# Kernel tuning notes

Hardware: AMD Instinct MI355X
Metric: run time of the kernel (lower is better)

## Reference

```python
import jax, jax.numpy as jnp
import numpy as np

B, S, H, I, E, TOP_K = 2, 1024, 1024, 2048, 8, 2


def setup_inputs() -> dict:
    key = jax.random.key(0)
    ks = jax.random.split(key, 5)
    return {
        "hidden_states": jax.random.normal(ks[0], (B, S, H), jnp.float32),
        # torch Linear weights are (out, in)
        "router_w": jax.random.normal(ks[1], (E, H), jnp.float32) * 0.02,
        "w1": jax.random.normal(ks[2], (E, I, H), jnp.float32) * 0.02,
        "v": jax.random.normal(ks[3], (E, I, H), jnp.float32) * 0.02,
        "w2": jax.random.normal(ks[4], (E, H, I), jnp.float32) * 0.02,
    }


def _moe(x, router_w, w1, v, w2):
    # x: [T, H] flattened tokens
    T = x.shape[0]
    n_exp = router_w.shape[0]
    logits = x @ router_w.T                                    # [T, E]
    probs = jax.nn.softmax(logits.astype(jnp.float32), axis=-1)
    top_p, top_i = jax.lax.top_k(probs, TOP_K)                 # [T, K]
    top_p = top_p / top_p.sum(axis=-1, keepdims=True)
    top_p = top_p.astype(x.dtype)
    # dense gate matrix [T, E]; zero for unselected experts -> identical math
    # to the torch gather / index_add combine
    gates = jnp.zeros((T, n_exp), x.dtype).at[
        jnp.arange(T)[:, None], top_i].set(top_p)
    out = jnp.zeros_like(x)
    for e in range(n_exp):  # small fixed expert loop keeps peak memory low
        h = jax.nn.gelu(x @ w1[e].T, approximate=False) * (x @ v[e].T)  # [T, I]
        out = out + gates[:, e:e + 1] * (h @ w2[e].T)                   # [T, H]
    return out, logits


def reference(hidden_states, router_w, w1, v, w2):
    b, s, h = hidden_states.shape
    out, logits = _moe(hidden_states.reshape(-1, h), router_w, w1, v, w2)
    return out.reshape(b, s, h), logits
```

## Files before the change

### kernel.cpp

```cpp
#include <hip/hip_runtime.h>
#include <math.h>

#define T 2048
#define HD 1024
#define ID 2048
#define NE 8
#define CSTRIDE 32

typedef short bf16x8 __attribute__((ext_vector_type(8)));
typedef float f32x4 __attribute__((ext_vector_type(4)));
typedef unsigned short u16x4 __attribute__((ext_vector_type(4)));

__device__ __forceinline__ unsigned short f2bf(float f) {
  union { float f; unsigned u; } v; v.f = f;
  unsigned r = v.u + 0x7FFFu + ((v.u >> 16) & 1u);
  return (unsigned short)(r >> 16);
}

__device__ __forceinline__ void cast_chunk16(const float* __restrict__ s,
                                             unsigned short* __restrict__ d,
                                             size_t base) {
  size_t o = base + (size_t)threadIdx.x * 4;
#pragma unroll
  for (int k = 0; k < 4; k++) {
    float4 f = *(const float4*)(s + o + k * 1024);
    u16x4 h;
    h[0] = f2bf(f.x); h[1] = f2bf(f.y); h[2] = f2bf(f.z); h[3] = f2bf(f.w);
    *(u16x4*)(d + o + k * 1024) = h;
  }
}

__device__ __forceinline__ void glds16(const unsigned short* g, unsigned short* l) {
  __builtin_amdgcn_global_load_lds(
      (const __attribute__((address_space(1))) unsigned int*)(g),
      (__attribute__((address_space(3))) unsigned int*)(l), 16, 0, 0);
}

__global__ __launch_bounds__(256) void prep_kernel(
    const float* __restrict__ x, const float* __restrict__ rw,
    const float* __restrict__ w1, const float* __restrict__ v,
    unsigned short* __restrict__ xb, unsigned short* __restrict__ w1b,
    unsigned short* __restrict__ vb, float* __restrict__ logits_out,
    int* __restrict__ pair_rowid, float* __restrict__ pair_gate,
    int* __restrict__ counts) {
  int bx = blockIdx.x;
  if (bx >= 768) {
    int cid = bx - 768;
    const float* s = (cid < 4096) ? w1 : v;
    unsigned short* d = (cid < 4096) ? w1b : vb;
    cast_chunk16(s, d, (size_t)(cid & 4095) * 4096);
    return;
  }
  if (bx >= 256) {
    cast_chunk16(x, xb, (size_t)(bx - 256) * 4096);
    return;
  }
  __shared__ int s_e[16];
  __shared__ int s_rid[16];
  __shared__ float s_gt[16];
  int tid = threadIdx.x;
  int wid = tid >> 6, lane = tid & 63;
  for (int tk = 0; tk < 2; ++tk) {
    int t = bx * 8 + wid * 2 + tk;
    float acc[NE];
#pragma unroll
    for (int e = 0; e < NE; e++) acc[e] = 0.f;
    const float* xrow = x + (size_t)t * HD;
#pragma unroll 2
    for (int j = 0; j < HD; j += 64) {
      float xv = xrow[j + lane];
#pragma unroll
      for (int e = 0; e < NE; e++) acc[e] += xv * rw[e * HD + j + lane];
    }
#pragma unroll
    for (int e = 0; e < NE; e++)
      for (int off = 32; off > 0; off >>= 1) acc[e] += __shfl_xor(acc[e], off, 64);
    if (lane == 0) {
#pragma unroll
      for (int e = 0; e < NE; e++) logits_out[t * NE + e] = acc[e];
      int e0 = 0;
#pragma unroll
      for (int e = 1; e < NE; e++) if (acc[e] > acc[e0]) e0 = e;
      int e1 = (e0 == 0) ? 1 : 0;
#pragma unroll
      for (int e = 0; e < NE; e++)
        if (e != e0 && e != e1 && acc[e] > acc[e1]) e1 = e;
      float b = __expf(acc[e1] - acc[e0]);
      float g0 = 1.f / (1.f + b);
      float g1 = 1.f - g0;
      int slot = (wid * 2 + tk) * 2;
      s_e[slot] = e0; s_rid[slot] = t * 2;     s_gt[slot] = g0;
      s_e[slot + 1] = e1; s_rid[slot + 1] = t * 2 + 1; s_gt[slot + 1] = g1;
    }
  }
  __syncthreads();
  if (tid < NE) {
    int cnt = 0;
#pragma unroll
    for (int k = 0; k < 16; k++) if (s_e[k] == tid) cnt++;
    if (cnt) {
      int base = atomicAdd(&counts[tid * CSTRIDE], cnt);
      int p = 0;
      for (int k = 0; k < 16; k++)
        if (s_e[k] == tid) {
          pair_rowid[tid * T + base + p] = s_rid[k];
          pair_gate[tid * T + base + p] = s_gt[k];
          p++;
        }
    }
  }
}

__global__ __launch_bounds__(256) void gemm1_kernel(
    const unsigned short* __restrict__ xb, const unsigned short* __restrict__ w1b,
    const unsigned short* __restrict__ vb, unsigned short* __restrict__ hb,
    const float* __restrict__ w2, unsigned short* __restrict__ w2b,
    const int* __restrict__ pair_rowid, const int* __restrict__ counts) {
  if (blockIdx.x >= 32) {
    int cid = (blockIdx.x - 32) + 32 * (blockIdx.y + 16 * blockIdx.z);
    cast_chunk16(w2, w2b, (size_t)cid * 4096);
    return;
  }
  int e = blockIdx.z;
  int cnt = counts[e * CSTRIDE];
  int row0 = blockIdx.y * 128;
  if (row0 >= cnt) return;
  __shared__ unsigned short As[128 * 64];
  __shared__ unsigned short B1s[64 * 64];
  __shared__ unsigned short B2s[64 * 64];
  __shared__ int rids[128];
  int tid = threadIdx.x;
  if (tid < 128) {
    int idx = row0 + tid; if (idx > cnt - 1) idx = cnt - 1;
    rids[tid] = pair_rowid[e * T + idx];
  }
  __syncthreads();
  int lane = tid & 63, wid = tid >> 6;
  int wr = wid >> 1, wc = wid & 1;
  int col0 = blockIdx.x * 64;
  int gr = lane >> 3, gc = lane & 7;
  const unsigned short *aA[4], *aB1[2], *aB2[2];
#pragma unroll
  for (int c = 0; c < 4; c++) {
    int row = (c * 4 + wid) * 8 + gr;
    int tok = rids[row] >> 1;
    aA[c] = xb + (size_t)tok * HD + ((gc ^ (row & 7)) * 8);
  }
#pragma unroll
  for (int c = 0; c < 2; c++) {
    int row = (c * 4 + wid) * 8 + gr;
    int kswz = ((gc ^ (row & 7)) * 8);
    aB1[c] = w1b + ((size_t)(e * ID + col0 + row)) * HD + kswz;
    aB2[c] = vb  + ((size_t)(e * ID + col0 + row)) * HD + kswz;
  }
  f32x4 acc1[4][2] = {};
  f32x4 acc3[4][2] = {};
  int mrow = lane & 15, kq = lane >> 4;
  int swzm = mrow & 7;
  for (int kt = 0; kt < HD; kt += 64) {
#pragma unroll
    for (int c = 0; c < 4; c++)
      glds16(aA[c] + kt, &As[(c * 4 + wid) * 512]);
#pragma unroll
    for (int c = 0; c < 2; c++) {
      glds16(aB1[c] + kt, &B1s[(c * 4 + wid) * 512]);
      glds16(aB2[c] + kt, &B2s[(c * 4 + wid) * 512]);
    }
    __syncthreads();
#pragma unroll
    for (int kk = 0; kk < 2; kk++) {
      int g = kk * 4 + kq;
      int ko = ((g ^ swzm) * 8);
      bf16x8 a[4], b1[2], b2[2];
#pragma unroll
      for (int mi = 0; mi < 4; mi++)
        a[mi] = *(const bf16x8*)&As[(wr * 64 + mi * 16 + mrow) * 64 + ko];
#pragma unroll
      for (int ni = 0; ni < 2; ni++) {
        b1[ni] = *(const bf16x8*)&B1s[(wc * 32 + ni * 16 + mrow) * 64 + ko];
        b2[ni] = *(const bf16x8*)&B2s[(wc * 32 + ni * 16 + mrow) * 64 + ko];
      }
#pragma unroll
      for (int mi = 0; mi < 4; mi++)
#pragma unroll
        for (int ni = 0; ni < 2; ni++) {
          acc1[mi][ni] = __builtin_amdgcn_mfma_f32_16x16x32_bf16(a[mi], b1[ni], acc1[mi][ni], 0, 0, 0);
          acc3[mi][ni] = __builtin_amdgcn_mfma_f32_16x16x32_bf16(a[mi], b2[ni], acc3[mi][ni], 0, 0, 0);
        }
    }
    __syncthreads();
  }
  int dcol = lane & 15, drow4 = (lane >> 4) * 4;
#pragma unroll
  for (int mi = 0; mi < 4; mi++)
#pragma unroll
    for (int ni = 0; ni < 2; ni++)
#pragma unroll
      for (int r = 0; r < 4; r++) {
        int lr = wr * 64 + mi * 16 + drow4 + r;
        if (row0 + lr < cnt) {
          float g1v = acc1[mi][ni][r];
          float g3v = acc3[mi][ni][r];
          float hval = 0.5f * g1v * (1.f + erff(g1v * 0.70710678118654752f)) * g3v;
          int rowid = rids[lr];
          hb[(size_t)rowid * ID + col0 + wc * 32 + ni * 16 + dcol] = f2bf(hval);
        }
      }
}

__global__ __launch_bounds__(256) void gemm2_kernel(
    const unsigned short* __restrict__ hb, const unsigned short* __restrict__ w2b,
    float* __restrict__ yb, const int* __restrict__ pair_rowid,
    const float* __restrict__ pair_gate, const int* __restrict__ counts) {
  int e = blockIdx.z >> 1, kh = blockIdx.z & 1;
  int cnt = counts[e * CSTRIDE];
  int row0 = blockIdx.y * 128;
  if (row0 >= cnt) return;
  __shared__ unsigned short As[128 * 64];
  __shared__ unsigned short B1s[64 * 64];
  __shared__ unsigned short B2s[64 * 64];
  __shared__ int rids[128];
  __shared__ float gts[128];
  int tid = threadIdx.x;
  if (tid < 128) {
    int idx = row0 + tid; if (idx > cnt - 1) idx = cnt - 1;
    rids[tid] = pair_rowid[e * T + idx];
    gts[tid] = pair_gate[e * T + idx];
  }
  __syncthreads();
  int lane = tid & 63, wid = tid >> 6;
  int wr = wid >> 1, wc = wid & 1;
  int col0 = blockIdx.x * 128;
  int gr = lane >> 3, gc = lane & 7;
  const unsigned short *aA[4], *aB1[2], *aB2[2];
#pragma unroll
  for (int c = 0; c < 4; c++) {
    int row = (c * 4 + wid) * 8 + gr;
    aA[c] = hb + (size_t)rids[row] * ID + kh * 1024 + ((gc ^ (row & 7)) * 8);
  }
#pragma unroll
  for (int c = 0; c < 2; c++) {
    int row = (c * 4 + wid) * 8 + gr;
    int kswz = ((gc ^ (row & 7)) * 8);
    aB1[c] = w2b + ((size_t)(e * HD + col0 + row)) * ID + kh * 1024 + kswz;
    aB2[c] = w2b + ((size_t)(e * HD + col0 + 64 + row)) * ID + kh * 1024 + kswz;
  }
  f32x4 acc1[4][2] = {};
  f32x4 acc3[4][2] = {};
  int mrow = lane & 15, kq = lane >> 4;
  int swzm = mrow & 7;
  for (int kt = 0; kt < 1024; kt += 64) {
#pragma unroll
    for (int c = 0; c < 4; c++)
      glds16(aA[c] + kt, &As[(c * 4 + wid) * 512]);
#pragma unroll
    for (int c = 0; c < 2; c++) {
      glds16(aB1[c] + kt, &B1s[(c * 4 + wid) * 512]);
      glds16(aB2[c] + kt, &B2s[(c * 4 + wid) * 512]);
    }
    __syncthreads();
#pragma unroll
    for (int kk = 0; kk < 2; kk++) {
      int g = kk * 4 + kq;
      int ko = ((g ^ swzm) * 8);
      bf16x8 a[4], b1[2], b2[2];
#pragma unroll
      for (int mi = 0; mi < 4; mi++)
        a[mi] = *(const bf16x8*)&As[(wr * 64 + mi * 16 + mrow) * 64 + ko];
#pragma unroll
      for (int ni = 0; ni < 2; ni++) {
        b1[ni] = *(const bf16x8*)&B1s[(wc * 32 + ni * 16 + mrow) * 64 + ko];
        b2[ni] = *(const bf16x8*)&B2s[(wc * 32 + ni * 16 + mrow) * 64 + ko];
      }
#pragma unroll
      for (int mi = 0; mi < 4; mi++)
#pragma unroll
        for (int ni = 0; ni < 2; ni++) {
          acc1[mi][ni] = __builtin_amdgcn_mfma_f32_16x16x32_bf16(a[mi], b1[ni], acc1[mi][ni], 0, 0, 0);
          acc3[mi][ni] = __builtin_amdgcn_mfma_f32_16x16x32_bf16(a[mi], b2[ni], acc3[mi][ni], 0, 0, 0);
        }
    }
    __syncthreads();
  }
  int dcol = lane & 15, drow4 = (lane >> 4) * 4;
  float* ybh = yb + (size_t)kh * (2 * T) * HD;
#pragma unroll
  for (int mi = 0; mi < 4; mi++)
#pragma unroll
    for (int ni = 0; ni < 2; ni++)
#pragma unroll
      for (int r = 0; r < 4; r++) {
        int lr = wr * 64 + mi * 16 + drow4 + r;
        if (row0 + lr < cnt) {
          size_t rbase = (size_t)rids[lr] * HD + col0 + wc * 32 + ni * 16 + dcol;
          ybh[rbase] = gts[lr] * acc1[mi][ni][r];
          ybh[rbase + 64] = gts[lr] * acc3[mi][ni][r];
        }
      }
}

__global__ __launch_bounds__(256) void combine_kernel(
    const float* __restrict__ yb, float* __restrict__ out) {
  size_t t = blockIdx.x;
  int c = threadIdx.x * 4;
  const size_t S = (size_t)(2 * T) * HD;
  float4 a0 = *(const float4*)(yb + (t * 2) * HD + c);
  float4 b0 = *(const float4*)(yb + (t * 2 + 1) * HD + c);
  float4 a1 = *(const float4*)(yb + S + (t * 2) * HD + c);
  float4 b1 = *(const float4*)(yb + S + (t * 2 + 1) * HD + c);
  float4 o;
  o.x = a0.x + b0.x + a1.x + b1.x;
  o.y = a0.y + b0.y + a1.y + b1.y;
  o.z = a0.z + b0.z + a1.z + b1.z;
  o.w = a0.w + b0.w + a1.w + b1.w;
  *(float4*)(out + t * HD + c) = o;
}

extern "C" void kernel_launch(void* const* d_in, const int* in_sizes, int n_in,
                              void* d_out, int out_size, void* d_ws, size_t ws_size,
                              hipStream_t stream) {
  const float* x  = (const float*)d_in[0];
  const float* rw = (const float*)d_in[1];
  const float* w1 = (const float*)d_in[2];
  const float* v  = (const float*)d_in[3];
  const float* w2 = (const float*)d_in[4];
  float* out = (float*)d_out;
  float* logits_out = out + (size_t)T * HD;

  char* ws = (char*)d_ws;
  unsigned short* xb  = (unsigned short*)(ws);
  unsigned short* hb  = (unsigned short*)(ws + (4u << 20));
  unsigned short* w1b = (unsigned short*)(ws + (20u << 20));
  unsigned short* vb  = (unsigned short*)(ws + (52u << 20));
  unsigned short* w2b = (unsigned short*)(ws + (84u << 20));
  float* yb           = (float*)(ws + (20u << 20));
  int*   pair_rowid   = (int*)  (ws + (116u << 20));
  float* pair_gate    = (float*)(ws + (116u << 20) + 65536);
  int*   counts       = (int*)  (ws + (116u << 20) + 131072);

  hipMemsetAsync(counts, 0, NE * CSTRIDE * sizeof(int), stream);

  prep_kernel<<<8960, 256, 0, stream>>>(x, rw, w1, v, xb, w1b, vb,
                                        logits_out, pair_rowid, pair_gate,
                                        counts);
  gemm1_kernel<<<dim3(ID / 64 + 32, T / 128, NE), 256, 0, stream>>>(
      xb, w1b, vb, hb, w2, w2b, pair_rowid, counts);
  gemm2_kernel<<<dim3(HD / 128, T / 128, NE * 2), 256, 0, stream>>>(
      hb, w2b, yb, pair_rowid, pair_gate, counts);
  combine_kernel<<<T, 256, 0, stream>>>(yb, out);
}
```

Before: 323.2 us.

## Fuse w2 fp32-to-bf16 cast into gemm2 LDS load path

Drops the separate w2 cast blocks from gemm1 along with the bf16 w2 workspace. gemm2 now streams fp32 w2 tiles straight into LDS with a swizzled layout and converts them to bf16 when building the MFMA operands. This removes one full write and read of the converted w2 weights. In exchange it doubles the w2 bytes moved per tile and the LDS footprint, and it repeats the conversion in every row-tile block that reuses the same w2 tile.

```diff
diff --git a/kernel.cpp b/kernel.cpp
--- a/kernel.cpp
+++ b/kernel.cpp
@@ -10,11 +10,21 @@
 typedef short bf16x8 __attribute__((ext_vector_type(8)));
 typedef float f32x4 __attribute__((ext_vector_type(4)));
 typedef unsigned short u16x4 __attribute__((ext_vector_type(4)));
+typedef unsigned short u16x8 __attribute__((ext_vector_type(8)));
 
 __device__ __forceinline__ unsigned short f2bf(float f) {
   union { float f; unsigned u; } v; v.f = f;
   unsigned r = v.u + 0x7FFFu + ((v.u >> 16) & 1u);
   return (unsigned short)(r >> 16);
+}
+
+union bfcast { u16x8 u; bf16x8 b; };
+
+__device__ __forceinline__ bf16x8 cvt8b(float4 a, float4 b) {
+  bfcast o;
+  o.u[0] = f2bf(a.x); o.u[1] = f2bf(a.y); o.u[2] = f2bf(a.z); o.u[3] = f2bf(a.w);
+  o.u[4] = f2bf(b.x); o.u[5] = f2bf(b.y); o.u[6] = f2bf(b.z); o.u[7] = f2bf(b.w);
+  return o.b;
 }
 
 __device__ __forceinline__ void cast_chunk16(const float* __restrict__ s,
@@ -31,6 +41,11 @@
 }
 
 __device__ __forceinline__ void glds16(const unsigned short* g, unsigned short* l) {
+  __builtin_amdgcn_global_load_lds(
+      (const __attribute__((address_space(1))) unsigned int*)(g),
+      (__attribute__((address_space(3))) unsigned int*)(l), 16, 0, 0);
+}
+__device__ __forceinline__ void glds16f(const float* g, float* l) {
   __builtin_amdgcn_global_load_lds(
       (const __attribute__((address_space(1))) unsigned int*)(g),
       (__attribute__((address_space(3))) unsigned int*)(l), 16, 0, 0);
@@ -114,13 +129,7 @@
 __global__ __launch_bounds__(256) void gemm1_kernel(
     const unsigned short* __restrict__ xb, const unsigned short* __restrict__ w1b,
     const unsigned short* __restrict__ vb, unsigned short* __restrict__ hb,
-    const float* __restrict__ w2, unsigned short* __restrict__ w2b,
     const int* __restrict__ pair_rowid, const int* __restrict__ counts) {
-  if (blockIdx.x >= 32) {
-    int cid = (blockIdx.x - 32) + 32 * (blockIdx.y + 16 * blockIdx.z);
-    cast_chunk16(w2, w2b, (size_t)cid * 4096);
-    return;
-  }
   int e = blockIdx.z;
   int cnt = counts[e * CSTRIDE];
   int row0 = blockIdx.y * 128;
@@ -209,7 +218,7 @@
 }
 
 __global__ __launch_bounds__(256) void gemm2_kernel(
-    const unsigned short* __restrict__ hb, const unsigned short* __restrict__ w2b,
+    const unsigned short* __restrict__ hb, const float* __restrict__ w2,
     float* __restrict__ yb, const int* __restrict__ pair_rowid,
     const float* __restrict__ pair_gate, const int* __restrict__ counts) {
   int e = blockIdx.z >> 1, kh = blockIdx.z & 1;
@@ -217,8 +226,8 @@
   int row0 = blockIdx.y * 128;
   if (row0 >= cnt) return;
   __shared__ unsigned short As[128 * 64];
-  __shared__ unsigned short B1s[64 * 64];
-  __shared__ unsigned short B2s[64 * 64];
+  __shared__ float B1f[64 * 64];
+  __shared__ float B2f[64 * 64];
   __shared__ int rids[128];
   __shared__ float gts[128];
   int tid = threadIdx.x;
@@ -232,18 +241,21 @@
   int wr = wid >> 1, wc = wid & 1;
   int col0 = blockIdx.x * 128;
   int gr = lane >> 3, gc = lane & 7;
-  const unsigned short *aA[4], *aB1[2], *aB2[2];
+  const unsigned short* aA[4];
+  const float *aB1[4], *aB2[4];
 #pragma unroll
   for (int c = 0; c < 4; c++) {
     int row = (c * 4 + wid) * 8 + gr;
     aA[c] = hb + (size_t)rids[row] * ID + kh * 1024 + ((gc ^ (row & 7)) * 8);
   }
 #pragma unroll
-  for (int c = 0; c < 2; c++) {
-    int row = (c * 4 + wid) * 8 + gr;
-    int kswz = ((gc ^ (row & 7)) * 8);
-    aB1[c] = w2b + ((size_t)(e * HD + col0 + row)) * ID + kh * 1024 + kswz;
-    aB2[c] = w2b + ((size_t)(e * HD + col0 + 64 + row)) * ID + kh * 1024 + kswz;
+  for (int c = 0; c < 4; c++) {
+    int rb = wid * 16 + c * 4;
+    int r = rb + (lane >> 4);
+    int c32 = (lane & 15) >> 1;
+    int k0 = ((c32 ^ (r & 7)) * 8) + (lane & 1) * 4;
+    aB1[c] = w2 + ((size_t)(e * HD + col0 + r)) * ID + kh * 1024 + k0;
+    aB2[c] = w2 + ((size_t)(e * HD + col0 + 64 + r)) * ID + kh * 1024 + k0;
   }
   f32x4 acc1[4][2] = {};
   f32x4 acc3[4][2] = {};
@@ -254,9 +266,9 @@
     for (int c = 0; c < 4; c++)
       glds16(aA[c] + kt, &As[(c * 4 + wid) * 512]);
 #pragma unroll
-    for (int c = 0; c < 2; c++) {
-      glds16(aB1[c] + kt, &B1s[(c * 4 + wid) * 512]);
-      glds16(aB2[c] + kt, &B2s[(c * 4 + wid) * 512]);
+    for (int c = 0; c < 4; c++) {
+      glds16f(aB1[c] + kt, &B1f[(wid * 16 + c * 4) * 64]);
+      glds16f(aB2[c] + kt, &B2f[(wid * 16 + c * 4) * 64]);
     }
     __syncthreads();
 #pragma unroll
@@ -269,8 +281,10 @@
         a[mi] = *(const bf16x8*)&As[(wr * 64 + mi * 16 + mrow) * 64 + ko];
 #pragma unroll
       for (int ni = 0; ni < 2; ni++) {
-        b1[ni] = *(const bf16x8*)&B1s[(wc * 32 + ni * 16 + mrow) * 64 + ko];
-        b2[ni] = *(const bf16x8*)&B2s[(wc * 32 + ni * 16 + mrow) * 64 + ko];
+        int rr = wc * 32 + ni * 16 + mrow;
+        int fo = rr * 64 + ko;
+        b1[ni] = cvt8b(*(const float4*)&B1f[fo], *(const float4*)&B1f[fo + 4]);
+        b2[ni] = cvt8b(*(const float4*)&B2f[fo], *(const float4*)&B2f[fo + 4]);
       }
 #pragma unroll
       for (int mi = 0; mi < 4; mi++)
@@ -332,7 +346,6 @@
   unsigned short* hb  = (unsigned short*)(ws + (4u << 20));
   unsigned short* w1b = (unsigned short*)(ws + (20u << 20));
   unsigned short* vb  = (unsigned short*)(ws + (52u << 20));
-  unsigned short* w2b = (unsigned short*)(ws + (84u << 20));
   float* yb           = (float*)(ws + (20u << 20));
   int*   pair_rowid   = (int*)  (ws + (116u << 20));
   float* pair_gate    = (float*)(ws + (116u << 20) + 65536);
@@ -343,9 +356,9 @@
   prep_kernel<<<8960, 256, 0, stream>>>(x, rw, w1, v, xb, w1b, vb,
                                         logits_out, pair_rowid, pair_gate,
                                         counts);
-  gemm1_kernel<<<dim3(ID / 64 + 32, T / 128, NE), 256, 0, stream>>>(
-      xb, w1b, vb, hb, w2, w2b, pair_rowid, counts);
+  gemm1_kernel<<<dim3(ID / 64, T / 128, NE), 256, 0, stream>>>(
+      xb, w1b, vb, hb, pair_rowid, counts);
   gemm2_kernel<<<dim3(HD / 128, T / 128, NE * 2), 256, 0, stream>>>(
-      hb, w2b, yb, pair_rowid, pair_gate, counts);
+      hb, w2, yb, pair_rowid, pair_gate, counts);
   combine_kernel<<<T, 256, 0, stream>>>(yb, out);
 }
```

Result: slower. 339.3 us (+5.0%).
